# Kernel optimization log

Hardware: AMD Instinct MI355X
Metric: run time of the kernel (lower is better)

Reference implementation:

```python
import jax, jax.numpy as jnp
import numpy as np

B, S, D, K, N = 4, 4096, 768, 24, 8192

def setup_inputs() -> dict:
    key = jax.random.key(0)
    k1, k2, k3, k4 = jax.random.split(key, 4)
    x = jax.random.normal(k1, (B, S, D), dtype=jnp.float32)
    phi = jax.random.normal(k2, (S, K), dtype=jnp.float32)
    M_inputs = jax.random.normal(k3, (D, D), dtype=jnp.float32) / np.sqrt(D)
    M_filters = jax.random.normal(k4, (K, D), dtype=jnp.float32) / np.sqrt(K)
    return {"x": x, "phi": phi, "M_inputs": M_inputs, "M_filters": M_filters, "n": N}


def reference(x, phi, M_inputs, M_filters, n):
    # STU.forward with use_approx=True, use_flash_fft=False
    bsz, sl, d = x.shape
    x_proj = x @ M_inputs               # [B, S, D]
    phi_proj = phi @ M_filters          # [S, D]
    # alternating sign sequence for the 'minus' spectral branch
    sgn = jnp.ones((1, sl, 1), dtype=x.dtype).at[:, 1::2].set(-1.0)
    # filters: [1, S, D, 1] broadcast over the plus/minus stack
    v = phi_proj[None, :, :, None]
    V = jnp.fft.rfft(v, n=n, axis=1)    # [1, n//2+1, D, 1] complex
    U = jnp.stack([x_proj, x_proj * sgn], axis=-1)  # [B, S, D, 2]
    Uf = jnp.fft.rfft(U, n=n, axis=1)   # [B, n//2+1, D, 2]
    U_conv = jnp.fft.irfft(V * Uf, n=n, axis=1)[:, :sl]  # [B, S, D, 2]
    spectral_plus = U_conv[..., 0]
    spectral_minus = U_conv[..., 1] * sgn
    return spectral_plus + spectral_minus
```

## Files before the change

### kernel.cpp

```cpp
#include <hip/hip_runtime.h>
#include <hip/hip_bf16.h>


#define NB 4
#define NS 4096
#define ND 768
#define NK 24

typedef __attribute__((ext_vector_type(8))) short short8;
typedef __attribute__((ext_vector_type(4))) float f32x4;
typedef __attribute__((ext_vector_type(4))) unsigned short u16x4;

static __device__ __forceinline__ float bf2f(unsigned short u) {
  union { unsigned int i; float f; } v; v.i = ((unsigned int)u) << 16; return v.f;
}
static __device__ __forceinline__ unsigned short f2bf(float f) {
  union { float f; unsigned int i; } v; v.f = f;
  return (unsigned short)((v.i + 0x7fffu + ((v.i >> 16) & 1u)) >> 16);
}

__device__ __forceinline__ float2 cadd(float2 a, float2 b){ return make_float2(a.x+b.x, a.y+b.y); }
__device__ __forceinline__ float2 csub(float2 a, float2 b){ return make_float2(a.x-b.x, a.y-b.y); }
__device__ __forceinline__ float2 cmul(float2 a, float2 b){ return make_float2(a.x*b.x-a.y*b.y, a.x*b.y+a.y*b.x); }
__device__ __forceinline__ float2 cmulc(float2 a, float2 b){ return make_float2(a.x*b.x+a.y*b.y, a.y*b.x-a.x*b.y); }

#define C4 0.70710678118654752f
#define C8 0.92387953251128674f
#define S8 0.38268343236508977f
#define TWO_PI 6.28318530717958648f

__device__ __forceinline__ void fft16_dif(float2 v[16]) {
  const float twr[8] = {1.f, C8, C4, S8, 0.f, -S8, -C4, -C8};
  const float twi[8] = {0.f, -S8, -C4, -C8, -1.f, -C8, -C4, -S8};
#pragma unroll
  for (int i = 0; i < 8; ++i) {
    float2 a = v[i], b = v[i+8];
    v[i] = cadd(a, b);
    float2 d = csub(a, b);
    v[i+8] = make_float2(d.x*twr[i]-d.y*twi[i], d.x*twi[i]+d.y*twr[i]);
  }
#pragma unroll
  for (int blk = 0; blk < 16; blk += 8)
#pragma unroll
    for (int i = 0; i < 4; ++i) {
      float2 a = v[blk+i], b = v[blk+i+4];
      v[blk+i] = cadd(a, b);
      float2 d = csub(a, b);
      v[blk+i+4] = make_float2(d.x*twr[2*i]-d.y*twi[2*i], d.x*twi[2*i]+d.y*twr[2*i]);
    }
#pragma unroll
  for (int blk = 0; blk < 16; blk += 4) {
    { float2 a = v[blk],   b = v[blk+2]; v[blk] = cadd(a,b);   v[blk+2] = csub(a,b); }
    { float2 a = v[blk+1], b = v[blk+3]; float2 d = csub(a,b);
      v[blk+1] = cadd(a,b); v[blk+3] = make_float2(d.y, -d.x); }
  }
#pragma unroll
  for (int blk = 0; blk < 16; blk += 2) {
    float2 a = v[blk], b = v[blk+1];
    v[blk] = cadd(a, b); v[blk+1] = csub(a, b);
  }
}

__device__ __forceinline__ void fft16_dif_zero8(float2 v[16]) {
  const float twr[8] = {1.f, C8, C4, S8, 0.f, -S8, -C4, -C8};
  const float twi[8] = {0.f, -S8, -C4, -C8, -1.f, -C8, -C4, -S8};
#pragma unroll
  for (int i = 1; i < 8; ++i) {
    float2 a = v[i];
    v[i+8] = make_float2(a.x*twr[i]-a.y*twi[i], a.x*twi[i]+a.y*twr[i]);
  }
  v[8] = v[0];
#pragma unroll
  for (int blk = 0; blk < 16; blk += 8)
#pragma unroll
    for (int i = 0; i < 4; ++i) {
      float2 a = v[blk+i], b = v[blk+i+4];
      v[blk+i] = cadd(a, b);
      float2 d = csub(a, b);
      v[blk+i+4] = make_float2(d.x*twr[2*i]-d.y*twi[2*i], d.x*twi[2*i]+d.y*twr[2*i]);
    }
#pragma unroll
  for (int blk = 0; blk < 16; blk += 4) {
    { float2 a = v[blk],   b = v[blk+2]; v[blk] = cadd(a,b);   v[blk+2] = csub(a,b); }
    { float2 a = v[blk+1], b = v[blk+3]; float2 d = csub(a,b);
      v[blk+1] = cadd(a,b); v[blk+3] = make_float2(d.y, -d.x); }
  }
#pragma unroll
  for (int blk = 0; blk < 16; blk += 2) {
    float2 a = v[blk], b = v[blk+1];
    v[blk] = cadd(a, b); v[blk+1] = csub(a, b);
  }
}

__device__ __forceinline__ void idft16(float2 v[16]) {
  const float twr[8] = {1.f, C8, C4, S8, 0.f, -S8, -C4, -C8};
  const float twi[8] = {0.f, S8, C4, C8, 1.f, C8, C4, S8};
#pragma unroll
  for (int blk = 0; blk < 16; blk += 2) {
    float2 a = v[blk], b = v[blk+1];
    v[blk] = cadd(a, b); v[blk+1] = csub(a, b);
  }
#pragma unroll
  for (int blk = 0; blk < 16; blk += 4) {
    { float2 a = v[blk],   b = v[blk+2]; v[blk] = cadd(a,b);   v[blk+2] = csub(a,b); }
    { float2 a = v[blk+1], b = v[blk+3]; float2 t = make_float2(-b.y, b.x);
      v[blk+1] = cadd(a,t); v[blk+3] = csub(a,t); }
  }
#pragma unroll
  for (int blk = 0; blk < 16; blk += 8)
#pragma unroll
    for (int i = 0; i < 4; ++i) {
      float2 b = v[blk+i+4];
      float2 t = make_float2(b.x*twr[2*i]-b.y*twi[2*i], b.x*twi[2*i]+b.y*twr[2*i]);
      float2 a = v[blk+i];
      v[blk+i] = cadd(a, t); v[blk+i+4] = csub(a, t);
    }
#pragma unroll
  for (int i = 0; i < 8; ++i) {
    float2 b = v[i+8];
    float2 t = make_float2(b.x*twr[i]-b.y*twi[i], b.x*twi[i]+b.y*twr[i]);
    float2 a = v[i];
    v[i] = cadd(a, t); v[i+8] = csub(a, t);
  }
}

__device__ __forceinline__ void idft16_low8(float2 v[16]) {
  const float twr[8] = {1.f, C8, C4, S8, 0.f, -S8, -C4, -C8};
  const float twi[8] = {0.f, S8, C4, C8, 1.f, C8, C4, S8};
#pragma unroll
  for (int blk = 0; blk < 16; blk += 2) {
    float2 a = v[blk], b = v[blk+1];
    v[blk] = cadd(a, b); v[blk+1] = csub(a, b);
  }
#pragma unroll
  for (int blk = 0; blk < 16; blk += 4) {
    { float2 a = v[blk],   b = v[blk+2]; v[blk] = cadd(a,b);   v[blk+2] = csub(a,b); }
    { float2 a = v[blk+1], b = v[blk+3]; float2 t = make_float2(-b.y, b.x);
      v[blk+1] = cadd(a,t); v[blk+3] = csub(a,t); }
  }
#pragma unroll
  for (int blk = 0; blk < 16; blk += 8)
#pragma unroll
    for (int i = 0; i < 4; ++i) {
      float2 b = v[blk+i+4];
      float2 t = make_float2(b.x*twr[2*i]-b.y*twi[2*i], b.x*twi[2*i]+b.y*twr[2*i]);
      float2 a = v[blk+i];
      v[blk+i] = cadd(a, t); v[blk+i+4] = csub(a, t);
    }
#pragma unroll
  for (int i = 0; i < 8; ++i) {
    float2 b = v[i+8];
    float2 t = make_float2(b.x*twr[i]-b.y*twi[i], b.x*twi[i]+b.y*twr[i]);
    v[i] = cadd(v[i], t);
  }
}

#define BR_TABLE {0,8,4,12,2,10,6,14,1,9,5,13,3,11,7,15}
#define PAD(i) ((i) + ((i) >> 4))

__global__ __launch_bounds__(256) void transpose_cast_Mi(const float* __restrict__ Mi,
                                                         unsigned short* __restrict__ MiT) {
  __shared__ float tile[64][65];
  const int d0 = blockIdx.x * 64;
  const int e0 = blockIdx.y * 64;
  const int tid = threadIdx.x;
#pragma unroll
  for (int i = 0; i < 16; ++i) {
    int ee = (tid >> 6) + i * 4;
    int dd = tid & 63;
    tile[ee][dd] = Mi[(e0 + ee) * ND + d0 + dd];
  }
  __syncthreads();
#pragma unroll
  for (int i = 0; i < 8; ++i) {
    int dd = (tid >> 5) + i * 8;
    int ee2 = (tid & 31) * 2;
    unsigned int w = (unsigned int)f2bf(tile[ee2][dd]) |
                     ((unsigned int)f2bf(tile[ee2 + 1][dd]) << 16);
    *(unsigned int*)(MiT + (size_t)(d0 + dd) * ND + e0 + ee2) = w;
  }
}

__global__ __launch_bounds__(256) void gemm_xprojT(const float* __restrict__ Xf,
                                                   const unsigned short* __restrict__ MiT,
                                                   unsigned short* __restrict__ XPT) {
  __shared__ __align__(16) unsigned char smem[24576];
  unsigned short* As0 = (unsigned short*)smem;
  unsigned short* Bs0 = (unsigned short*)(smem + 4096);
  unsigned short* As1 = (unsigned short*)(smem + 12288);
  unsigned short* Bs1 = (unsigned short*)(smem + 16384);

  const int tid = threadIdx.x;
  const int lane = tid & 63;
  const int wave = tid >> 6;
  const int f = blockIdx.x;
  const int swz = (f & 7) * 192 + (f >> 3);
  const int c0 = (swz % 6) * 128;
  const int r0 = (swz / 6) * 64;

  const int rowA = tid >> 2;
  const int kcA = tid & 3;
  const int wkA = ((kcA ^ ((tid >> 3) & 3)) * 8);
  const int rowB = lane >> 2;
  const int kcB = (((lane & 3) ^ ((lane >> 3) & 3)) * 8);

  f32x4 acc[2][4];
#pragma unroll
  for (int m = 0; m < 2; ++m)
#pragma unroll
    for (int n = 0; n < 4; ++n) acc[m][n] = (f32x4){0.f, 0.f, 0.f, 0.f};

  {
    const float* ga = Xf + (size_t)(r0 + rowA) * ND + kcA * 8;
    float4 p0 = *(const float4*)ga;
    float4 p1 = *(const float4*)(ga + 4);
#pragma unroll
    for (int h = 0; h < 2; ++h) {
      int c = wave * 2 + h;
      const unsigned short* gb = MiT + (size_t)(c0 + c * 16 + rowB) * ND + kcB;
      __builtin_amdgcn_global_load_lds(
          (const __attribute__((address_space(1))) void*)gb,
          (__attribute__((address_space(3))) void*)(Bs0 + c * 512), 16, 0, 0);
    }
    unsigned int w0 = (unsigned int)f2bf(p0.x) | ((unsigned int)f2bf(p0.y) << 16);
    unsigned int w1 = (unsigned int)f2bf(p0.z) | ((unsigned int)f2bf(p0.w) << 16);
    unsigned int w2 = (unsigned int)f2bf(p1.x) | ((unsigned int)f2bf(p1.y) << 16);
    unsigned int w3 = (unsigned int)f2bf(p1.z) | ((unsigned int)f2bf(p1.w) << 16);
    *(uint4*)(As0 + rowA * 32 + wkA) = make_uint4(w0, w1, w2, w3);
  }
  __syncthreads();

  const int wr = (wave >> 1) * 32;
  const int wc = (wave & 1) * 64;

  for (int t = 0; t < NK; ++t) {
    unsigned short* Ac = (t & 1) ? As1 : As0;
    unsigned short* Bc = (t & 1) ? Bs1 : Bs0;
    unsigned short* An = (t & 1) ? As0 : As1;
    unsigned short* Bn = (t & 1) ? Bs0 : Bs1;
    const bool pre = (t < NK - 1);
    float4 p0, p1;
    if (pre) {
      const int k0n = (t + 1) * 32;
      const float* ga = Xf + (size_t)(r0 + rowA) * ND + k0n + kcA * 8;
      p0 = *(const float4*)ga;
      p1 = *(const float4*)(ga + 4);
#pragma unroll
      for (int h = 0; h < 2; ++h) {
        int c = wave * 2 + h;
        const unsigned short* gb = MiT + (size_t)(c0 + c * 16 + rowB) * ND + k0n + kcB;
        __builtin_amdgcn_global_load_lds(
            (const __attribute__((address_space(1))) void*)gb,
            (__attribute__((address_space(3))) void*)(Bn + c * 512), 16, 0, 0);
      }
    }

    short8 a[2], b[4];
#pragma unroll
    for (int m = 0; m < 2; ++m) {
      int r = wr + m * 16 + (lane & 15);
      a[m] = *(const short8*)(Ac + r * 32 + (((lane >> 4) ^ ((r >> 1) & 3)) * 8));
    }
#pragma unroll
    for (int n = 0; n < 4; ++n) {
      int r = wc + n * 16 + (lane & 15);
      b[n] = *(const short8*)(Bc + r * 32 + (((lane >> 4) ^ ((r >> 1) & 3)) * 8));
    }
#pragma unroll
    for (int m = 0; m < 2; ++m)
#pragma unroll
      for (int n = 0; n < 4; ++n)
        acc[m][n] = __builtin_amdgcn_mfma_f32_16x16x32_bf16(a[m], b[n], acc[m][n], 0, 0, 0);

    if (pre) {
      unsigned int w0 = (unsigned int)f2bf(p0.x) | ((unsigned int)f2bf(p0.y) << 16);
      unsigned int w1 = (unsigned int)f2bf(p0.z) | ((unsigned int)f2bf(p0.w) << 16);
      unsigned int w2 = (unsigned int)f2bf(p1.x) | ((unsigned int)f2bf(p1.y) << 16);
      unsigned int w3 = (unsigned int)f2bf(p1.z) | ((unsigned int)f2bf(p1.w) << 16);
      *(uint4*)(An + rowA * 32 + wkA) = make_uint4(w0, w1, w2, w3);
      __syncthreads();
    }
  }
  __syncthreads();

  unsigned int* Cb = (unsigned int*)smem;
#pragma unroll
  for (int m = 0; m < 2; ++m)
#pragma unroll
    for (int n = 0; n < 4; ++n) {
      int col = wc + n * 16 + (lane & 15);
      int sp = (wr + m * 16 + (lane >> 4) * 4) >> 1;
      f32x4 a4 = acc[m][n];
      unsigned int w0 = (unsigned int)f2bf(a4[0]) | ((unsigned int)f2bf(a4[1]) << 16);
      unsigned int w1 = (unsigned int)f2bf(a4[2]) | ((unsigned int)f2bf(a4[3]) << 16);
      *(uint2*)(Cb + col * 34 + sp) = make_uint2(w0, w1);
    }
  __syncthreads();
  const int bI = r0 >> 12;
  const int sBase = r0 & (NS - 1);
  {
    int col = tid >> 1, half = tid & 1;
    const unsigned int* srcl = Cb + col * 34 + half * 16;
    unsigned int* dstg = (unsigned int*)(XPT + ((size_t)bI * ND + c0 + col) * NS + sBase) + half * 16;
#pragma unroll
    for (int k = 0; k < 4; ++k)
      *(uint4*)(dstg + k * 4) = *(const uint4*)(srcl + k * 4);
  }
}

__global__ __launch_bounds__(256) void filter_fft(const float* __restrict__ phi,
                                                  const float* __restrict__ Mf,
                                                  float2* __restrict__ Hbr) {
  __shared__ float LR[4352], LI[4352];
  __shared__ float2 TA[256], TB[256];
  const int d = blockIdx.x;
  const int tid = threadIdx.x;
  const int BR[16] = BR_TABLE;
  float2 v[16];

  {
    float sn, cs;
    __sincosf(-(TWO_PI / 4096.f) * (float)tid, &sn, &cs); TA[tid] = make_float2(cs, sn);
    __sincosf(-(TWO_PI / 256.f) * (float)tid, &sn, &cs);  TB[tid] = make_float2(cs, sn);
  }

  float mf[NK];
#pragma unroll
  for (int k = 0; k < NK; ++k) mf[k] = Mf[k * ND + d];
#pragma unroll
  for (int n2 = 0; n2 < 8; ++n2) {
    int m = n2 * 256 + tid;
    const float* pr = phi + (size_t)(2 * m) * NK;
    float acc = 0.f;
#pragma unroll
    for (int k = 0; k < NK; ++k) acc += pr[k] * mf[k];
    v[n2] = make_float2(acc, 0.f);
  }
#pragma unroll
  for (int n2 = 8; n2 < 16; ++n2) v[n2] = make_float2(0.f, 0.f);

  fft16_dif_zero8(v);
  __syncthreads();
  const int t1 = tid >> 4, t0 = tid & 15;
#pragma unroll
  for (int p = 1; p < 16; ++p) v[BR[p]] = cmul(v[BR[p]], cmul(TB[p * t1], TA[p * t0]));
#pragma unroll
  for (int r = 0; r < 16; ++r) { int i = BR[r] * 256 + tid; int s = PAD(i); LR[s] = v[r].x; LI[s] = v[r].y; }
  __syncthreads();

  const int p2 = tid >> 4, n0 = tid & 15;
#pragma unroll
  for (int n1 = 0; n1 < 16; ++n1) { int i = p2 * 256 + n1 * 16 + n0; int s = PAD(i); v[n1] = make_float2(LR[s], LI[s]); }
  fft16_dif(v);
#pragma unroll
  for (int p = 1; p < 16; ++p) v[BR[p]] = cmul(v[BR[p]], TB[p * n0]);
  __syncthreads();
#pragma unroll
  for (int r = 0; r < 16; ++r) { int i = p2 * 256 + BR[r] * 16 + n0; int s = PAD(i); LR[s] = v[r].x; LI[s] = v[r].y; }
  __syncthreads();

#pragma unroll
  for (int q = 0; q < 16; ++q) { int i = tid * 16 + q; int s = PAD(i); v[q] = make_float2(LR[s], LI[s]); }
  fft16_dif(v);
  const float sc = 2.0f / 4096.0f;
  float2* H = Hbr + (size_t)d * 4096;
#pragma unroll
  for (int r = 0; r < 16; ++r)
    H[r * 256 + tid] = make_float2(v[r].x * sc, v[r].y * sc);
}

__global__ __launch_bounds__(256) void conv_kernel(const unsigned short* __restrict__ XPT,
                                                   const float2* __restrict__ Hbr,
                                                   unsigned int* __restrict__ outTb) {
  __shared__ float LR[4352], LI[4352];
  __shared__ float2 TA[256], TB[256];
  const int bd = blockIdx.x;
  const int d = bd % ND;
  const int tid = threadIdx.x;
  const int BR[16] = BR_TABLE;
  float2 v[16];

  {
    float sn, cs;
    __sincosf(-(TWO_PI / 4096.f) * (float)tid, &sn, &cs); TA[tid] = make_float2(cs, sn);
    __sincosf(-(TWO_PI / 256.f) * (float)tid, &sn, &cs);  TB[tid] = make_float2(cs, sn);
  }

  const unsigned int* src = (const unsigned int*)(XPT + (size_t)bd * NS);
#pragma unroll
  for (int n2 = 0; n2 < 8; ++n2) {
    unsigned int w = src[n2 * 256 + tid];
    v[n2] = make_float2(bf2f((unsigned short)(w & 0xffffu)), bf2f((unsigned short)(w >> 16)));
  }
#pragma unroll
  for (int n2 = 8; n2 < 16; ++n2) v[n2] = make_float2(0.f, 0.f);

  fft16_dif_zero8(v);
  __syncthreads();
  const int t1 = tid >> 4, t0 = tid & 15;
#pragma unroll
  for (int p = 1; p < 16; ++p) v[BR[p]] = cmul(v[BR[p]], cmul(TB[p * t1], TA[p * t0]));
#pragma unroll
  for (int r = 0; r < 16; ++r) { int i = BR[r] * 256 + tid; int s = PAD(i); LR[s] = v[r].x; LI[s] = v[r].y; }
  __syncthreads();

  const int p2 = tid >> 4, n0 = tid & 15;
#pragma unroll
  for (int n1 = 0; n1 < 16; ++n1) { int i = p2 * 256 + n1 * 16 + n0; int s = PAD(i); v[n1] = make_float2(LR[s], LI[s]); }
  fft16_dif(v);
#pragma unroll
  for (int p = 1; p < 16; ++p) v[BR[p]] = cmul(v[BR[p]], TB[p * n0]);
  __syncthreads();
#pragma unroll
  for (int r = 0; r < 16; ++r) { int i = p2 * 256 + BR[r] * 16 + n0; int s = PAD(i); LR[s] = v[r].x; LI[s] = v[r].y; }
  __syncthreads();

#pragma unroll
  for (int q = 0; q < 16; ++q) { int i = tid * 16 + q; int s = PAD(i); v[q] = make_float2(LR[s], LI[s]); }
  fft16_dif(v);
  const float2* H = Hbr + (size_t)d * 4096;
#pragma unroll
  for (int r = 0; r < 16; ++r) v[r] = cmul(v[r], H[r * 256 + tid]);
  idft16(v);
#pragma unroll
  for (int n = 1; n < 16; ++n) v[n] = cmulc(v[n], TB[n * (tid & 15)]);
#pragma unroll
  for (int n = 0; n < 16; ++n) { int i = tid * 16 + n; int s = PAD(i); LR[s] = v[n].x; LI[s] = v[n].y; }
  __syncthreads();

#pragma unroll
  for (int r = 0; r < 16; ++r) { int i = p2 * 256 + BR[r] * 16 + n0; int s = PAD(i); v[r] = make_float2(LR[s], LI[s]); }
  idft16(v);
  {
    float2 cA = TA[p2 * n0];
#pragma unroll
    for (int n = 0; n < 16; ++n) v[n] = cmulc(v[n], cmul(TB[p2 * n], cA));
  }
  __syncthreads();
#pragma unroll
  for (int n = 0; n < 16; ++n) { int i = p2 * 256 + n * 16 + n0; int s = PAD(i); LR[s] = v[n].x; LI[s] = v[n].y; }
  __syncthreads();

#pragma unroll
  for (int r = 0; r < 16; ++r) { int i = BR[r] * 256 + tid; int s = PAD(i); v[r] = make_float2(LR[s], LI[s]); }
  idft16_low8(v);
  unsigned int* dst = outTb + (size_t)bd * 2048;
#pragma unroll
  for (int n2 = 0; n2 < 8; ++n2) {
    float2 y = v[n2];
    unsigned int w = (unsigned int)f2bf(y.x) | ((unsigned int)f2bf(y.y) << 16);
    dst[(n2 << 8) + tid] = w;
  }
}

__global__ __launch_bounds__(256) void transpose_out(const unsigned int* __restrict__ outTb,
                                                     float* __restrict__ out) {
  __shared__ float tile[64][65];
  const int b = blockIdx.z;
  const int d0 = blockIdx.y * 64;
  const int s0 = blockIdx.x * 64;
  const int tid = threadIdx.x;
#pragma unroll
  for (int i = 0; i < 8; ++i) {
    int dd = (tid >> 5) + i * 8;
    int ss2 = (tid & 31) * 2;
    unsigned int w = outTb[(((size_t)b * ND + d0 + dd) * NS + s0 + ss2) >> 1];
    tile[dd][ss2]     = bf2f((unsigned short)(w & 0xffffu));
    tile[dd][ss2 + 1] = bf2f((unsigned short)(w >> 16));
  }
  __syncthreads();
#pragma unroll
  for (int i = 0; i < 16; ++i) {
    int ss = (tid >> 6) + i * 4;
    int dd = tid & 63;
    out[((size_t)b * NS + s0 + ss) * ND + d0 + dd] = tile[dd][ss];
  }
}

extern "C" void kernel_launch(void* const* d_in, const int* in_sizes, int n_in,
                              void* d_out, int out_size, void* d_ws, size_t ws_size,
                              hipStream_t stream) {
  const float* x   = (const float*)d_in[0];
  const float* phi = (const float*)d_in[1];
  const float* Mi  = (const float*)d_in[2];
  const float* Mf  = (const float*)d_in[3];
  float* out = (float*)d_out;

  const size_t SZ_XPT = (size_t)NB * ND * NS * 2;
  const size_t SZ_HBR = (size_t)ND * 4096 * 8;
  const size_t SZ_POOL = (size_t)NB * ND * NS * 4;
  if (ws_size < SZ_XPT + SZ_HBR + SZ_POOL) return;

  char* ws = (char*)d_ws;
  unsigned short* xprojT = (unsigned short*)ws;
  float2* Hbr = (float2*)(ws + SZ_XPT);
  char* pool = ws + SZ_XPT + SZ_HBR;
  unsigned int* outTb = (unsigned int*)pool;
  unsigned short* MiT = (unsigned short*)(pool + 25165824);

  transpose_cast_Mi<<<dim3(ND / 64, ND / 64), 256, 0, stream>>>(Mi, MiT);
  gemm_xprojT<<<1536, 256, 0, stream>>>(x, MiT, xprojT);
  filter_fft<<<ND, 256, 0, stream>>>(phi, Mf, Hbr);
  conv_kernel<<<NB * ND, 256, 0, stream>>>(xprojT, Hbr, outTb);
  transpose_out<<<dim3(NS / 64, ND / 64, NB), 256, 0, stream>>>(outTb, out);
}
```

Before: 130.9 us.

## Load GEMM operand fragments directly from global memory, dropping LDS staging

Rewrites the x-projection GEMM main loop so that each wave loads its A (fp32, converted to bf16 in registers) and B (bf16) MFMA fragments straight from global memory, instead of staging them through double-buffered shared memory with per-iteration barriers. The goal is to remove the LDS writes and reads and the __syncthreads in the K loop. In exchange, operands are no longer shared through LDS, so each wave fetches redundant data from global memory or L2. The loop also no longer overlaps the next tile's loads with MFMA, relying instead on unroll-by-2 and hardware latency hiding. Shared memory is now used only for the output transpose buffer.

```diff
diff --git a/kernel.cpp b/kernel.cpp
--- a/kernel.cpp
+++ b/kernel.cpp
@@ -181,15 +181,19 @@
   }
 }
 
+static __device__ __forceinline__ short8 cvt8(float4 q0, float4 q1) {
+  short8 r;
+  r[0] = (short)f2bf(q0.x); r[1] = (short)f2bf(q0.y);
+  r[2] = (short)f2bf(q0.z); r[3] = (short)f2bf(q0.w);
+  r[4] = (short)f2bf(q1.x); r[5] = (short)f2bf(q1.y);
+  r[6] = (short)f2bf(q1.z); r[7] = (short)f2bf(q1.w);
+  return r;
+}
+
 __global__ __launch_bounds__(256) void gemm_xprojT(const float* __restrict__ Xf,
                                                    const unsigned short* __restrict__ MiT,
                                                    unsigned short* __restrict__ XPT) {
-  __shared__ __align__(16) unsigned char smem[24576];
-  unsigned short* As0 = (unsigned short*)smem;
-  unsigned short* Bs0 = (unsigned short*)(smem + 4096);
-  unsigned short* As1 = (unsigned short*)(smem + 12288);
-  unsigned short* Bs1 = (unsigned short*)(smem + 16384);
-
+  __shared__ __align__(16) unsigned int Cb[128 * 34];
   const int tid = threadIdx.x;
   const int lane = tid & 63;
   const int wave = tid >> 6;
@@ -198,92 +202,40 @@
   const int c0 = (swz % 6) * 128;
   const int r0 = (swz / 6) * 64;
 
-  const int rowA = tid >> 2;
-  const int kcA = tid & 3;
-  const int wkA = ((kcA ^ ((tid >> 3) & 3)) * 8);
-  const int rowB = lane >> 2;
-  const int kcB = (((lane & 3) ^ ((lane >> 3) & 3)) * 8);
-
-  f32x4 acc[2][4];
-#pragma unroll
-  for (int m = 0; m < 2; ++m)
-#pragma unroll
-    for (int n = 0; n < 4; ++n) acc[m][n] = (f32x4){0.f, 0.f, 0.f, 0.f};
-
-  {
-    const float* ga = Xf + (size_t)(r0 + rowA) * ND + kcA * 8;
-    float4 p0 = *(const float4*)ga;
-    float4 p1 = *(const float4*)(ga + 4);
-#pragma unroll
-    for (int h = 0; h < 2; ++h) {
-      int c = wave * 2 + h;
-      const unsigned short* gb = MiT + (size_t)(c0 + c * 16 + rowB) * ND + kcB;
-      __builtin_amdgcn_global_load_lds(
-          (const __attribute__((address_space(1))) void*)gb,
-          (__attribute__((address_space(3))) void*)(Bs0 + c * 512), 16, 0, 0);
-    }
-    unsigned int w0 = (unsigned int)f2bf(p0.x) | ((unsigned int)f2bf(p0.y) << 16);
-    unsigned int w1 = (unsigned int)f2bf(p0.z) | ((unsigned int)f2bf(p0.w) << 16);
-    unsigned int w2 = (unsigned int)f2bf(p1.x) | ((unsigned int)f2bf(p1.y) << 16);
-    unsigned int w3 = (unsigned int)f2bf(p1.z) | ((unsigned int)f2bf(p1.w) << 16);
-    *(uint4*)(As0 + rowA * 32 + wkA) = make_uint4(w0, w1, w2, w3);
-  }
-  __syncthreads();
-
   const int wr = (wave >> 1) * 32;
   const int wc = (wave & 1) * 64;
 
+  const int fr = lane & 15;
+  const int fk = (lane >> 4) * 8;
+  const float* pa = Xf + (size_t)(r0 + wr + fr) * ND + fk;
+  const unsigned short* pb = MiT + (size_t)(c0 + wc + fr) * ND + fk;
+
+  f32x4 acc[2][4];
+#pragma unroll
+  for (int m = 0; m < 2; ++m)
+#pragma unroll
+    for (int n = 0; n < 4; ++n) acc[m][n] = (f32x4){0.f, 0.f, 0.f, 0.f};
+
+#pragma unroll 2
   for (int t = 0; t < NK; ++t) {
-    unsigned short* Ac = (t & 1) ? As1 : As0;
-    unsigned short* Bc = (t & 1) ? Bs1 : Bs0;
-    unsigned short* An = (t & 1) ? As0 : As1;
-    unsigned short* Bn = (t & 1) ? Bs0 : Bs1;
-    const bool pre = (t < NK - 1);
-    float4 p0, p1;
-    if (pre) {
-      const int k0n = (t + 1) * 32;
-      const float* ga = Xf + (size_t)(r0 + rowA) * ND + k0n + kcA * 8;
-      p0 = *(const float4*)ga;
-      p1 = *(const float4*)(ga + 4);
-#pragma unroll
-      for (int h = 0; h < 2; ++h) {
-        int c = wave * 2 + h;
-        const unsigned short* gb = MiT + (size_t)(c0 + c * 16 + rowB) * ND + k0n + kcB;
-        __builtin_amdgcn_global_load_lds(
-            (const __attribute__((address_space(1))) void*)gb,
-            (__attribute__((address_space(3))) void*)(Bn + c * 512), 16, 0, 0);
-      }
-    }
-
     short8 a[2], b[4];
 #pragma unroll
     for (int m = 0; m < 2; ++m) {
-      int r = wr + m * 16 + (lane & 15);
-      a[m] = *(const short8*)(Ac + r * 32 + (((lane >> 4) ^ ((r >> 1) & 3)) * 8));
-    }
-#pragma unroll
-    for (int n = 0; n < 4; ++n) {
-      int r = wc + n * 16 + (lane & 15);
-      b[n] = *(const short8*)(Bc + r * 32 + (((lane >> 4) ^ ((r >> 1) & 3)) * 8));
-    }
+      const float* p = pa + (size_t)(m * 16) * ND + t * 32;
+      float4 q0 = *(const float4*)p;
+      float4 q1 = *(const float4*)(p + 4);
+      a[m] = cvt8(q0, q1);
+    }
+#pragma unroll
+    for (int n = 0; n < 4; ++n)
+      b[n] = *(const short8*)(pb + (size_t)(n * 16) * ND + t * 32);
 #pragma unroll
     for (int m = 0; m < 2; ++m)
 #pragma unroll
       for (int n = 0; n < 4; ++n)
         acc[m][n] = __builtin_amdgcn_mfma_f32_16x16x32_bf16(a[m], b[n], acc[m][n], 0, 0, 0);
-
-    if (pre) {
-      unsigned int w0 = (unsigned int)f2bf(p0.x) | ((unsigned int)f2bf(p0.y) << 16);
-      unsigned int w1 = (unsigned int)f2bf(p0.z) | ((unsigned int)f2bf(p0.w) << 16);
-      unsigned int w2 = (unsigned int)f2bf(p1.x) | ((unsigned int)f2bf(p1.y) << 16);
-      unsigned int w3 = (unsigned int)f2bf(p1.z) | ((unsigned int)f2bf(p1.w) << 16);
-      *(uint4*)(An + rowA * 32 + wkA) = make_uint4(w0, w1, w2, w3);
-      __syncthreads();
-    }
-  }
-  __syncthreads();
-
-  unsigned int* Cb = (unsigned int*)smem;
+  }
+
 #pragma unroll
   for (int m = 0; m < 2; ++m)
 #pragma unroll
```

Result: slower. 219.7 us (+67.8%).
